# Optimization experiments

Hardware: AMD Instinct MI355X
Metric: run time of the kernel (lower is better)

## Reference

```python
import jax, jax.numpy as jnp
import numpy as np

TEMPERATURE = 10000.0
LN_EPS = 1e-5

def build_freqs(H, W, head_dim):
    # (H*W, head_dim) rotary angles: [theta_h, theta_h, theta_w, theta_w]
    gh, gw = jnp.meshgrid(jnp.arange(H, dtype=jnp.float32), jnp.arange(W, dtype=jnp.float32), indexing='ij')
    dq = head_dim // 4
    freq = 1.0 / (TEMPERATURE ** (jnp.arange(dq, dtype=jnp.float32) / dq))
    th = gh.reshape(-1, 1) * freq[None, :]
    tw = gw.reshape(-1, 1) * freq[None, :]
    return jnp.concatenate([th, th, tw, tw], axis=-1)

def apply_rope(x, freqs):
    # x: (B, nh, N, hd), freqs: (N, hd)
    cos = jnp.cos(freqs)[None, None]
    sin = jnp.sin(freqs)[None, None]
    hd = x.shape[-1]
    x1, x2 = x[..., :hd // 2], x[..., hd // 2:]
    x_rot = jnp.concatenate([-x2, x1], axis=-1)
    return x * cos + x_rot * sin

def setup_inputs() -> dict:
    key = jax.random.key(0)
    ks = jax.random.split(key, 8)
    dim, hidden, B, H, W = 192, 384, 4, 128, 128
    N = H * W
    s = 0.02
    return {
        'x': jax.random.normal(ks[0], (B, N, dim), jnp.float32),
        'in_w': jax.random.normal(ks[1], (hidden, dim), jnp.float32) * s,
        'in_b': jnp.zeros((hidden,), jnp.float32),
        'qkv_w': jax.random.normal(ks[2], (3 * hidden, hidden), jnp.float32) * s,
        'qkv_b': jnp.zeros((3 * hidden,), jnp.float32),
        'lepe_w': jax.random.normal(ks[3], (hidden, 1, 3, 3), jnp.float32) * s,
        'lepe_b': jnp.zeros((hidden,), jnp.float32),
        'ln_g': jnp.ones((hidden,), jnp.float32),
        'ln_b': jnp.zeros((hidden,), jnp.float32),
        'out_w': jax.random.normal(ks[4], (dim, hidden), jnp.float32) * s,
        'out_b': jnp.zeros((dim,), jnp.float32),
        'H': H,
        'W': W,
    }

def reference(x, in_w, in_b, qkv_w, qkv_b, lepe_w, lepe_b, ln_g, ln_b, out_w, out_b, H, W):
    B, N, C = x.shape
    hidden = in_w.shape[0]
    nh = 8
    hd = hidden // nh
    # in_proj: 1x1 conv == per-token linear
    x_seq = jnp.einsum('bnc,hc->bnh', x, in_w) + in_b
    # fused qkv
    qkv = jnp.einsum('bnh,oh->bno', x_seq, qkv_w) + qkv_b
    q, k, v = jnp.split(qkv, 3, axis=-1)
    # LEPE: 3x3 depthwise conv on V in NCHW layout
    v2d = v.transpose(0, 2, 1).reshape(B, hidden, H, W)
    lepe = jax.lax.conv_general_dilated(
        v2d, lepe_w, window_strides=(1, 1), padding=((1, 1), (1, 1)),
        feature_group_count=hidden, dimension_numbers=('NCHW', 'OIHW', 'NCHW'))
    lepe = lepe + lepe_b[None, :, None, None]
    v = v + lepe.reshape(B, hidden, N).transpose(0, 2, 1)
    # split heads -> (B, nh, N, hd)
    q = q.reshape(B, N, nh, hd).transpose(0, 2, 1, 3)
    k = k.reshape(B, N, nh, hd).transpose(0, 2, 1, 3)
    v = v.reshape(B, N, nh, hd).transpose(0, 2, 1, 3)
    freqs = build_freqs(H, W, hd)
    q = apply_rope(q, freqs)
    k = apply_rope(k, freqs)
    # phi = ELU + 1 feature map
    q = jax.nn.elu(q) + 1.0
    k = jax.nn.elu(k) + 1.0
    # linear attention associativity trick
    kv = jnp.einsum('bhnd,bhne->bhde', k, v)
    out = jnp.einsum('bhnd,bhde->bhne', q, kv)
    k_sum = k.sum(axis=2)  # (B, nh, hd)
    denom = jnp.maximum(jnp.einsum('bhnd,bhd->bhn', q, k_sum)[..., None], 1e-6)
    out = out / denom
    out = out.transpose(0, 2, 1, 3).reshape(B, N, hidden)
    # LayerNorm + out_proj
    mu = out.mean(axis=-1, keepdims=True)
    var = out.var(axis=-1, keepdims=True)
    out = (out - mu) * jax.lax.rsqrt(var + LN_EPS) * ln_g + ln_b
    return jnp.einsum('bnh,ch->bnc', out, out_w) + out_b
```

## Files before the change

kernel.cpp:

```cpp
#include <hip/hip_runtime.h>
#include <cstdint>
#include <cstddef>

#define NN_TOK 16384
#define ROWS   65536
#define CDIM   192
#define HID    384
#define NHEAD  8
#define HD     48
#define QKVO   1152

typedef unsigned short ushort_t;
typedef __bf16 bf16x8 __attribute__((ext_vector_type(8)));
typedef float  f32x4  __attribute__((ext_vector_type(4)));

__device__ __forceinline__ ushort_t f2bf(float f) {
  __bf16 h = (__bf16)f;
  ushort_t u;
  __builtin_memcpy(&u, &h, 2);
  return u;
}
__device__ __forceinline__ float bf2f(ushort_t u) {
  return __uint_as_float(((unsigned int)u) << 16);
}

__global__ void cast_x(const float* __restrict__ x, ushort_t* __restrict__ xb, int n8) {
  int i = blockIdx.x * blockDim.x + threadIdx.x;
  if (i >= n8) return;
  const float4* src = (const float4*)(x + (size_t)i * 8);
  float4 f0 = src[0], f1 = src[1];
  uint4 pk;
  pk.x = (unsigned)f2bf(f0.x) | ((unsigned)f2bf(f0.y) << 16);
  pk.y = (unsigned)f2bf(f0.z) | ((unsigned)f2bf(f0.w) << 16);
  pk.z = (unsigned)f2bf(f1.x) | ((unsigned)f2bf(f1.y) << 16);
  pk.w = (unsigned)f2bf(f1.z) | ((unsigned)f2bf(f1.w) << 16);
  *(uint4*)(xb + (size_t)i * 8) = pk;
}

__global__ void combine_w(const float* __restrict__ in_w, const float* __restrict__ in_b,
                          const float* __restrict__ qkv_w, const float* __restrict__ qkv_b,
                          ushort_t* __restrict__ Wcb, float* __restrict__ bc) {
  int o = blockIdx.x;
  int c = threadIdx.x;
  const float* qw = qkv_w + o * HID;
  float s = 0.f;
  for (int m = 0; m < HID; ++m) s += qw[m] * in_w[m * CDIM + c];
  Wcb[o * CDIM + c] = f2bf(s);
  if (c == 0) {
    float sb = qkv_b[o];
    for (int m = 0; m < HID; ++m) sb += qw[m] * in_b[m];
    bc[o] = sb;
  }
}

__global__ void cast_owT(const float* __restrict__ w, ushort_t* __restrict__ wt, int n) {
  int i = blockIdx.x * blockDim.x + threadIdx.x;
  if (i >= n) return;
  int j = i & 7, rest = i >> 3;
  int l15 = rest & 15; rest >>= 4;
  int quad = rest & 3; rest >>= 2;
  int kt = rest % 12, ct = rest / 12;
  int col = ct * 16 + l15, k = kt * 32 + quad * 8 + j;
  wt[i] = f2bf(w[col * HID + k]);
}

__global__ void build_tab(float4* __restrict__ tab4) {
  int i = blockIdx.x * blockDim.x + threadIdx.x;
  if (i >= NN_TOK * 24) return;
  int n = i / 24, dp = i - n * 24;
  int j = dp % 12;
  const float c0 = 1.1073093649624542f;
  float freq = exp2f(-(float)j * c0);
  float fy = (float)(n >> 7), fx = (float)(n & 127);
  float s1, c1, s2, c2;
  sincosf(fy * freq, &s1, &c1);
  sincosf(fx * freq, &s2, &c2);
  tab4[i] = make_float4(c1, s1, c2, s2);
}

template<int BM, int BN, int WM, int WN>
__global__ __launch_bounds__(256) void gemm_qkv(const ushort_t* __restrict__ A, int lda,
                                                const ushort_t* __restrict__ Wb,
                                                const float* __restrict__ bias,
                                                ushort_t* __restrict__ qb,
                                                ushort_t* __restrict__ kTb,
                                                ushort_t* __restrict__ vTb,
                                                int K, int nbx) {
  constexpr int TM = BM / WM / 16;
  constexpr int TN = BN / WN / 16;
  __shared__ __align__(16) ushort_t As[BM][40];
  __shared__ __align__(16) ushort_t Bs[BN][40];
  const int t    = threadIdx.x;
  const int lane = t & 63;
  const int wave = t >> 6;
  const int quad = lane >> 4;
  const int l15  = lane & 15;
  const int wm   = wave / WN, wn = wave % WN;
  const int m_base = wm * (BM / WM);
  const int n_base = wn * (BN / WN);
  const int cpx = gridDim.x >> 3;
  const int id  = blockIdx.x;
  const int swz = (id & 7) * cpx + (id >> 3);
  const int o0  = (swz % nbx) * BN;
  const int n0  = (swz / nbx) * BM;
  f32x4 acc[TM][TN] = {};

  for (int kt = 0; kt < K; kt += 32) {
    for (int c = t; c < BM * 4; c += 256) {
      int row = c >> 2, col8 = (c & 3) * 8;
      *(uint4*)&As[row][col8] = *(const uint4*)(A + (size_t)(n0 + row) * lda + kt + col8);
    }
    for (int c = t; c < BN * 4; c += 256) {
      int row = c >> 2, col8 = (c & 3) * 8;
      *(uint4*)&Bs[row][col8] = *(const uint4*)(Wb + (size_t)(o0 + row) * K + kt + col8);
    }
    __syncthreads();
    bf16x8 af[TM], bfr[TN];
#pragma unroll
    for (int mi = 0; mi < TM; ++mi)
      af[mi] = *(const bf16x8*)&As[m_base + mi * 16 + l15][quad * 8];
#pragma unroll
    for (int ni = 0; ni < TN; ++ni)
      bfr[ni] = *(const bf16x8*)&Bs[n_base + ni * 16 + l15][quad * 8];
#pragma unroll
    for (int mi = 0; mi < TM; ++mi)
#pragma unroll
      for (int ni = 0; ni < TN; ++ni)
        acc[mi][ni] = __builtin_amdgcn_mfma_f32_16x16x32_bf16(af[mi], bfr[ni], acc[mi][ni], 0, 0, 0);
    __syncthreads();
  }
#pragma unroll
  for (int mi = 0; mi < TM; ++mi) {
#pragma unroll
    for (int ni = 0; ni < TN; ++ni) {
      int col = o0 + n_base + ni * 16 + l15;
      float bv = bias[col];
      int rbase = n0 + m_base + mi * 16 + quad * 4;
      if (col < HID) {
#pragma unroll
        for (int r = 0; r < 4; ++r)
          qb[(size_t)(rbase + r) * HID + col] = f2bf(acc[mi][ni][r] + bv);
      } else {
        int co = col - HID;
        ushort_t* dp = kTb;
        if (co >= HID) { co -= HID; dp = vTb; }
        int hh = co / 48, dd = co - hh * 48;
#pragma unroll
        for (int r = 0; r < 4; ++r) {
          int row = rbase + r;
          int bb = row >> 14, n = row & (NN_TOK - 1);
          dp[((size_t)(bb * 8 + hh) * NN_TOK + n) * 48 + dd] = f2bf(acc[mi][ni][r] + bv);
        }
      }
    }
  }
}

__device__ __forceinline__ int fragEl(int pg, int nb, int dd, int nm) {
  return pg * 2200 + nb * 136 + dd * 8 + nm;
}

__global__ __launch_bounds__(256) void kv_partial_k(const ushort_t* __restrict__ kq,
                                                    const ushort_t* __restrict__ vq,
                                                    const float4* __restrict__ tab4,
                                                    const float* __restrict__ lw,
                                                    const float* __restrict__ lb,
                                                    float* __restrict__ part) {
  const int bid   = blockIdx.x;
  const int chunk = bid & 63;
  const int bh    = bid >> 6;
  const int h     = bh & 7;
  const int t     = threadIdx.x;
  const int lane  = t & 63;
  const int wave  = t >> 6;
  __shared__ __align__(16) ushort_t ksR[3 * 2200];
  __shared__ __align__(16) ushort_t vsR[4 * 2200];
  __shared__ __align__(16) float wlds[9][48];
  __shared__ __align__(16) float blds[48];
  float* red = (float*)&ksR[0];
  for (int c = t; c < 432; c += 256) {
    int ch = c / 9, tap = c - ch * 9;
    wlds[tap][ch] = lw[(h * HD + ch) * 9 + tap];
  }
  if (t < 48) blds[t] = lb[h * HD + t];
  for (int c = t; c < 2048; c += 256) {
    int nb = c >> 7, dd = (c >> 3) & 15, nm = c & 7;
    vsR[fragEl(3, nb, dd, nm)] = (dd == 0) ? (ushort_t)0x3F80 : (ushort_t)0;
  }
  __syncthreads();

  const int g  = lane >> 4;
  const int d0 = lane & 15;
  f32x4 acc[3][4] = {};
  const size_t hbase = (size_t)bh * NN_TOK * 48;
  const int nst0 = chunk * 256;

  for (int it = 0; it < 2; ++it) {
    const int nbase = it * 128;
    for (int c = t; c < 384; c += 256) {
      int rr = c / 3, s8 = (c - (c / 3) * 3) * 8;
      int nl = nst0 + nbase + rr;
      const ushort_t* kr = kq + hbase + (size_t)nl * 48;
      uint4 ka = *(const uint4*)(kr + s8);
      uint4 kb = *(const uint4*)(kr + s8 + 24);
      ushort_t ua[8], ub[8];
      *(uint4*)ua = ka; *(uint4*)ub = kb;
      const float4* t4 = tab4 + nl * 24 + s8;
      const int nb = rr >> 3, nm = rr & 7;
#pragma unroll
      for (int jj = 0; jj < 8; ++jj) {
        float4 cs = t4[jj];
        float in1 = bf2f(ua[jj]), in2 = bf2f(ub[jj]);
        float o1 = in1 * cs.x - in2 * cs.y;
        float o2 = in2 * cs.z + in1 * cs.w;
        o1 = (o1 > 0.f) ? o1 + 1.f : __expf(o1);
        o2 = (o2 > 0.f) ? o2 + 1.f : __expf(o2);
        const int d1 = s8 + jj, d2 = s8 + 24 + jj;
        ksR[fragEl(d1 >> 4, nb, d1 & 15, nm)] = f2bf(o1);
        ksR[fragEl(d2 >> 4, nb, d2 & 15, nm)] = f2bf(o2);
      }
    }
    {
      const int y = (nst0 + nbase) >> 7;
      for (int c = t; c < 768; c += 256) {
        int rr = c / 6, gg = c - (c / 6) * 6;
        int x = rr;
        float a8[8], ctr[8];
        *(float4*)&a8[0] = *(const float4*)&blds[gg * 8];
        *(float4*)&a8[4] = *(const float4*)&blds[gg * 8 + 4];
#pragma unroll
        for (int dy = -1; dy <= 1; ++dy) {
#pragma unroll
          for (int dx = -1; dx <= 1; ++dx) {
            int yy = y + dy, xx = x + dx;
            bool inb = ((unsigned)yy < 128u) && ((unsigned)xx < 128u);
            int yc = min(max(yy, 0), 127), xc = min(max(xx, 0), 127);
            const ushort_t* src = vq + hbase + (size_t)((yc << 7) + xc) * 48 + gg * 8;
            uint4 pk = *(const uint4*)src;
            if (!inb) pk = make_uint4(0u, 0u, 0u, 0u);
            const int tap = (dy + 1) * 3 + (dx + 1);
            float wt[8];
            *(float4*)&wt[0] = *(const float4*)&wlds[tap][gg * 8];
            *(float4*)&wt[4] = *(const float4*)&wlds[tap][gg * 8 + 4];
            ushort_t uu[8];
            *(uint4*)uu = pk;
#pragma unroll
            for (int ci = 0; ci < 8; ++ci) {
              float val = bf2f(uu[ci]);
              if (dy == 0 && dx == 0) ctr[ci] = val;
              a8[ci] += wt[ci] * val;
            }
          }
        }
        const int nb = rr >> 3, nm = rr & 7;
#pragma unroll
        for (int ci = 0; ci < 8; ++ci) {
          const int e = gg * 8 + ci;
          vsR[fragEl(e >> 4, nb, e & 15, nm)] = f2bf(ctr[ci] + a8[ci]);
        }
      }
    }
    __syncthreads();
    {
      const int w4 = wave * 4 + g;
      bf16x8 af[3], bfr[4];
#pragma unroll
      for (int dg = 0; dg < 3; ++dg) af[dg]  = *(const bf16x8*)&ksR[fragEl(dg, w4, d0, 0)];
#pragma unroll
      for (int eg = 0; eg < 4; ++eg) bfr[eg] = *(const bf16x8*)&vsR[fragEl(eg, w4, d0, 0)];
#pragma unroll
      for (int dg = 0; dg < 3; ++dg)
#pragma unroll
        for (int eg = 0; eg < 4; ++eg)
          acc[dg][eg] = __builtin_amdgcn_mfma_f32_16x16x32_bf16(af[dg], bfr[eg], acc[dg][eg], 0, 0, 0);
    }
    __syncthreads();
  }
  if (wave == 0) {
#pragma unroll
    for (int dg = 0; dg < 3; ++dg)
#pragma unroll
      for (int eg = 0; eg < 4; ++eg)
#pragma unroll
        for (int r = 0; r < 4; ++r)
          red[(dg * 16 + g * 4 + r) * 64 + eg * 16 + d0] = acc[dg][eg][r];
  }
  __syncthreads();
  for (int w = 1; w < 4; ++w) {
    if (wave == w) {
#pragma unroll
      for (int dg = 0; dg < 3; ++dg)
#pragma unroll
        for (int eg = 0; eg < 4; ++eg)
#pragma unroll
          for (int r = 0; r < 4; ++r)
            red[(dg * 16 + g * 4 + r) * 64 + eg * 16 + d0] += acc[dg][eg][r];
    }
    __syncthreads();
  }
  float* p = part + (size_t)bid * 2352;
  for (int c = t; c < 2352; c += 256) {
    int d = c / 49, e = c - d * 49;
    p[c] = red[d * 64 + e];
  }
}

__global__ void kv_phase2(const float* __restrict__ part, ushort_t* __restrict__ kvT) {
  int bh  = blockIdx.x >> 3;
  int seg = blockIdx.x & 7;
  int t   = threadIdx.x;
  ushort_t* dst = kvT + (size_t)bh * 8192;
  for (int i = seg * 1024 + t; i < (seg + 1) * 1024; i += 256) {
    int rem = i & 4095, e = rem >> 6, d = rem & 63;
    if (d >= 48 || e >= 49) dst[i] = 0;
  }
  int cend = (seg + 1) * 294;
  for (int c = seg * 294 + t; c < cend; c += 256) {
    const float* p = part + (size_t)(bh * 64) * 2352 + c;
    float s = 0.f;
    for (int ch = 0; ch < 64; ++ch) s += p[(size_t)ch * 2352];
    int d = c / 49, e = c - d * 49;
    ushort_t hi = f2bf(s);
    float lo = s - bf2f(hi);
    dst[(size_t)e * 64 + d]        = hi;
    dst[4096 + (size_t)e * 64 + d] = f2bf(lo);
  }
}

__global__ __launch_bounds__(256) void attn_ln_fused(const ushort_t* __restrict__ qb,
                                                     const float4* __restrict__ tab4,
                                                     const ushort_t* __restrict__ kvT,
                                                     const float* __restrict__ ln_g,
                                                     const float* __restrict__ ln_b,
                                                     const ushort_t* __restrict__ owbT,
                                                     const float* __restrict__ out_b,
                                                     float* __restrict__ outp) {
  __shared__ __align__(16) ushort_t qsL[32][392];
  __shared__ __align__(16) float tabL[32][100];
  __shared__ float lnp[4][32][2];
  const int t    = threadIdx.x;
  const int lane = t & 63;
  const int wave = t >> 6;
  const int quad = lane >> 4;
  const int l15  = lane & 15;
  const int row0 = blockIdx.x * 32;
  const int b    = row0 >> 14;
  const int h0   = wave * 2;

  for (int c = t; c < 1536; c += 256) {
    int r = c / 48, seg = c - (c / 48) * 48;
    *(uint4*)&qsL[r][seg * 8] = *(const uint4*)(qb + (size_t)(row0 + r) * HID + seg * 8);
  }
  for (int c = t; c < 768; c += 256) {
    int r = c / 24, dp = c - (c / 24) * 24;
    float4 v = tab4[(size_t)(((row0 + r) & (NN_TOK - 1))) * 24 + dp];
    *(float4*)&tabL[r][dp * 4] = v;
  }
  __syncthreads();

  f32x4 acc[2][2][4] = {};

  float gg[2][3], bb[2][3];
#pragma unroll
  for (int hi = 0; hi < 2; ++hi)
#pragma unroll
    for (int nt = 0; nt < 3; ++nt) {
      int col = (h0 + hi) * 48 + nt * 16 + l15;
      gg[hi][nt] = ln_g[col];
      bb[hi][nt] = ln_b[col];
    }

#pragma unroll
  for (int s = 0; s < 2; ++s) {
    const int d0 = s * 32 + quad * 8;
    bf16x8 bfH[2][4], bfL[2][4];
#pragma unroll
    for (int hi = 0; hi < 2; ++hi) {
      const ushort_t* kb = kvT + (size_t)(b * 8 + h0 + hi) * 8192;
#pragma unroll
      for (int nt = 0; nt < 4; ++nt) {
        bfH[hi][nt] = *(const bf16x8*)(kb + (nt * 16 + l15) * 64 + d0);
        bfL[hi][nt] = *(const bf16x8*)(kb + 4096 + (nt * 16 + l15) * 64 + d0);
      }
    }
    const bool valid = d0 < 48;
    const bool caseA = d0 < 24;
    const int dp0 = caseA ? d0 : d0 - 24;
    bf16x8 af[2][2] = {};
    if (valid) {
      const int dpart = caseA ? d0 + 24 : d0 - 24;
      const int csel  = caseA ? 0 : 2;
      const float sgn = caseA ? -1.f : 1.f;
#pragma unroll
      for (int m = 0; m < 2; ++m) {
        const int r = m * 16 + l15;
        float2 cs[8];
#pragma unroll
        for (int j = 0; j < 8; ++j)
          cs[j] = *(const float2*)&tabL[r][(dp0 + j) * 4 + csel];
#pragma unroll
        for (int hi = 0; hi < 2; ++hi) {
          const ushort_t* qr = &qsL[r][(h0 + hi) * 48];
          uint4 pr = *(const uint4*)(qr + d0);
          uint4 pa = *(const uint4*)(qr + dpart);
          ushort_t up[8], ua[8];
          *(uint4*)up = pr; *(uint4*)ua = pa;
          bf16x8 av;
#pragma unroll
          for (int j = 0; j < 8; ++j) {
            float vp = bf2f(up[j]), va = bf2f(ua[j]);
            float o = vp * cs[j].x + va * (sgn * cs[j].y);
            o = (o > 0.f) ? o + 1.f : __expf(o);
            av[j] = (__bf16)o;
          }
          af[hi][m] = av;
        }
      }
    }
#pragma unroll
    for (int hi = 0; hi < 2; ++hi)
#pragma unroll
      for (int nt = 0; nt < 4; ++nt)
#pragma unroll
        for (int m = 0; m < 2; ++m) {
          acc[hi][m][nt] = __builtin_amdgcn_mfma_f32_16x16x32_bf16(af[hi][m], bfH[hi][nt], acc[hi][m][nt], 0, 0, 0);
          acc[hi][m][nt] = __builtin_amdgcn_mfma_f32_16x16x32_bf16(af[hi][m], bfL[hi][nt], acc[hi][m][nt], 0, 0, 0);
        }
  }

  float rdn[2][2][4];
#pragma unroll
  for (int hi = 0; hi < 2; ++hi)
#pragma unroll
    for (int m = 0; m < 2; ++m)
#pragma unroll
      for (int r = 0; r < 4; ++r) {
        float dn = __shfl(acc[hi][m][3][r], lane & 48);
        rdn[hi][m][r] = 1.f / fmaxf(dn, 1e-6f);
      }
  float s1[2][4] = {}, s2[2][4] = {};
#pragma unroll
  for (int hi = 0; hi < 2; ++hi)
#pragma unroll
    for (int m = 0; m < 2; ++m)
#pragma unroll
      for (int nt = 0; nt < 3; ++nt)
#pragma unroll
        for (int r = 0; r < 4; ++r) {
          float o = acc[hi][m][nt][r] * rdn[hi][m][r];
          acc[hi][m][nt][r] = o;
          s1[m][r] += o;
          s2[m][r] += o * o;
        }
#pragma unroll
  for (int m = 0; m < 2; ++m)
#pragma unroll
    for (int r = 0; r < 4; ++r) {
#pragma unroll
      for (int msk = 1; msk < 16; msk <<= 1) {
        s1[m][r] += __shfl_xor(s1[m][r], msk, 64);
        s2[m][r] += __shfl_xor(s2[m][r], msk, 64);
      }
    }
  if (l15 == 0) {
#pragma unroll
    for (int m = 0; m < 2; ++m)
#pragma unroll
      for (int r = 0; r < 4; ++r) {
        int rr = m * 16 + quad * 4 + r;
        lnp[wave][rr][0] = s1[m][r];
        lnp[wave][rr][1] = s2[m][r];
      }
  }
  __syncthreads();
  float muv[2][4], rsv[2][4];
#pragma unroll
  for (int m = 0; m < 2; ++m)
#pragma unroll
    for (int r = 0; r < 4; ++r) {
      int rr = m * 16 + quad * 4 + r;
      float a  = lnp[0][rr][0] + lnp[1][rr][0] + lnp[2][rr][0] + lnp[3][rr][0];
      float bq = lnp[0][rr][1] + lnp[1][rr][1] + lnp[2][rr][1] + lnp[3][rr][1];
      float mu  = a * (1.f / 384.f);
      float var = bq * (1.f / 384.f) - mu * mu;
      muv[m][r] = mu;
      rsv[m][r] = rsqrtf(var + 1e-5f);
    }
#pragma unroll
  for (int hi = 0; hi < 2; ++hi)
#pragma unroll
    for (int m = 0; m < 2; ++m)
#pragma unroll
      for (int nt = 0; nt < 3; ++nt) {
        int col = (h0 + hi) * 48 + nt * 16 + l15;
#pragma unroll
        for (int r = 0; r < 4; ++r) {
          int rr = m * 16 + quad * 4 + r;
          float v = (acc[hi][m][nt][r] - muv[m][r]) * rsv[m][r] * gg[hi][nt] + bb[hi][nt];
          qsL[rr][col] = f2bf(v);
        }
      }
  __syncthreads();

  f32x4 oac[2][3] = {};
  const int ct0 = wave * 3;
  float obv[3];
#pragma unroll
  for (int nt = 0; nt < 3; ++nt) obv[nt] = out_b[ct0 * 16 + nt * 16 + l15];
#pragma unroll
  for (int kt = 0; kt < 12; ++kt) {
    bf16x8 af2[2];
    af2[0] = *(const bf16x8*)&qsL[l15][kt * 32 + quad * 8];
    af2[1] = *(const bf16x8*)&qsL[16 + l15][kt * 32 + quad * 8];
    bf16x8 bfr2[3];
#pragma unroll
    for (int nt = 0; nt < 3; ++nt)
      bfr2[nt] = *(const bf16x8*)&owbT[(size_t)((((ct0 + nt) * 12 + kt) * 4 + quad) * 16 + l15) * 8];
#pragma unroll
    for (int m2 = 0; m2 < 2; ++m2)
#pragma unroll
      for (int nt = 0; nt < 3; ++nt)
        oac[m2][nt] = __builtin_amdgcn_mfma_f32_16x16x32_bf16(af2[m2], bfr2[nt], oac[m2][nt], 0, 0, 0);
  }
  __syncthreads();
  float* coL = (float*)&qsL[0][0];
#pragma unroll
  for (int m2 = 0; m2 < 2; ++m2)
#pragma unroll
    for (int nt = 0; nt < 3; ++nt) {
      int col = ct0 * 16 + nt * 16 + l15;
#pragma unroll
      for (int r = 0; r < 4; ++r)
        coL[(m2 * 16 + quad * 4 + r) * 196 + col] = oac[m2][nt][r] + obv[nt];
    }
  __syncthreads();
  for (int c = t; c < 1536; c += 256) {
    int r = c / 48, seg = c - (c / 48) * 48;
    *(float4*)(outp + (size_t)(row0 + r) * CDIM + seg * 4) = *(const float4*)&coL[r * 196 + seg * 4];
  }
}

extern "C" void kernel_launch(void* const* d_in, const int* in_sizes, int n_in,
                              void* d_out, int out_size, void* d_ws, size_t ws_size,
                              hipStream_t stream) {
  const float* x      = (const float*)d_in[0];
  const float* in_w   = (const float*)d_in[1];
  const float* in_b   = (const float*)d_in[2];
  const float* qkv_w  = (const float*)d_in[3];
  const float* qkv_b  = (const float*)d_in[4];
  const float* lepe_w = (const float*)d_in[5];
  const float* lepe_b = (const float*)d_in[6];
  const float* ln_g   = (const float*)d_in[7];
  const float* ln_b   = (const float*)d_in[8];
  const float* out_w  = (const float*)d_in[9];
  const float* out_b  = (const float*)d_in[10];
  float* out = (float*)d_out;

  float*    ws     = (float*)d_ws;
  float*    qbF    = ws;
  float*    kTF    = qbF  + (size_t)ROWS * HID / 2;
  float*    vTF    = kTF  + (size_t)ROWS * HID / 2;
  float*    xbF    = vTF  + (size_t)ROWS * HID / 2;
  float*    WcbF   = xbF  + (size_t)ROWS * CDIM / 2;
  float*    bc     = WcbF + (size_t)QKVO * CDIM / 2;
  float*    owbF   = bc   + QKVO;
  float*    tab4F  = owbF + (size_t)CDIM * HID / 2;
  ushort_t* qb     = (ushort_t*)qbF;
  ushort_t* kTb    = (ushort_t*)kTF;
  ushort_t* vTb    = (ushort_t*)vTF;
  ushort_t* xb     = (ushort_t*)xbF;
  float*    part   = xbF;
  ushort_t* kvT    = (ushort_t*)(xbF + (size_t)2048 * 2352);
  ushort_t* Wcb    = (ushort_t*)WcbF;
  ushort_t* owbT   = (ushort_t*)owbF;
  float4*   tab4   = (float4*)tab4F;

  cast_x<<<(ROWS * CDIM / 8 + 255) / 256, 256, 0, stream>>>(x, xb, ROWS * CDIM / 8);
  combine_w<<<QKVO, CDIM, 0, stream>>>(in_w, in_b, qkv_w, qkv_b, Wcb, bc);
  cast_owT<<<(CDIM * HID + 255) / 256, 256, 0, stream>>>(out_w, owbT, CDIM * HID);
  build_tab<<<(NN_TOK * 24 + 255) / 256, 256, 0, stream>>>(tab4);

  gemm_qkv<128, 128, 2, 2><<<4608, 256, 0, stream>>>(
      xb, CDIM, Wcb, bc, qb, kTb, vTb, CDIM, 9);

  kv_partial_k<<<2048, 256, 0, stream>>>(kTb, vTb, tab4, lepe_w, lepe_b, part);
  kv_phase2<<<256, 256, 0, stream>>>(part, kvT);

  attn_ln_fused<<<ROWS / 32, 256, 0, stream>>>(qb, tab4, kvT, ln_g, ln_b, owbT, out_b, out);
}
```

Before: 382.8 us.

## Merge prep kernels into one launch and raise wave priority around MFMA loops

Four small preprocessing kernels (x cast, weight combine, out_w transpose cast, rope table) become one kernel that dispatches on block index, cutting three launches and their inter-kernel gaps. The MFMA inner loops in the GEMM, kv-partial, attention and out-projection kernels are also wrapped with s_setprio(1)/s_setprio(0) to favour waves issuing matrix ops. The merged kernel uses 256 threads for the combine_w part where only 192 are active, and setprio may change wave interleaving in either direction.

```diff
diff --git a/kernel.cpp b/kernel.cpp
--- a/kernel.cpp
+++ b/kernel.cpp
@@ -24,58 +24,62 @@
   return __uint_as_float(((unsigned int)u) << 16);
 }
 
-__global__ void cast_x(const float* __restrict__ x, ushort_t* __restrict__ xb, int n8) {
-  int i = blockIdx.x * blockDim.x + threadIdx.x;
-  if (i >= n8) return;
-  const float4* src = (const float4*)(x + (size_t)i * 8);
-  float4 f0 = src[0], f1 = src[1];
-  uint4 pk;
-  pk.x = (unsigned)f2bf(f0.x) | ((unsigned)f2bf(f0.y) << 16);
-  pk.y = (unsigned)f2bf(f0.z) | ((unsigned)f2bf(f0.w) << 16);
-  pk.z = (unsigned)f2bf(f1.x) | ((unsigned)f2bf(f1.y) << 16);
-  pk.w = (unsigned)f2bf(f1.z) | ((unsigned)f2bf(f1.w) << 16);
-  *(uint4*)(xb + (size_t)i * 8) = pk;
-}
-
-__global__ void combine_w(const float* __restrict__ in_w, const float* __restrict__ in_b,
-                          const float* __restrict__ qkv_w, const float* __restrict__ qkv_b,
-                          ushort_t* __restrict__ Wcb, float* __restrict__ bc) {
-  int o = blockIdx.x;
-  int c = threadIdx.x;
-  const float* qw = qkv_w + o * HID;
-  float s = 0.f;
-  for (int m = 0; m < HID; ++m) s += qw[m] * in_w[m * CDIM + c];
-  Wcb[o * CDIM + c] = f2bf(s);
-  if (c == 0) {
-    float sb = qkv_b[o];
-    for (int m = 0; m < HID; ++m) sb += qw[m] * in_b[m];
-    bc[o] = sb;
-  }
-}
-
-__global__ void cast_owT(const float* __restrict__ w, ushort_t* __restrict__ wt, int n) {
-  int i = blockIdx.x * blockDim.x + threadIdx.x;
-  if (i >= n) return;
-  int j = i & 7, rest = i >> 3;
-  int l15 = rest & 15; rest >>= 4;
-  int quad = rest & 3; rest >>= 2;
-  int kt = rest % 12, ct = rest / 12;
-  int col = ct * 16 + l15, k = kt * 32 + quad * 8 + j;
-  wt[i] = f2bf(w[col * HID + k]);
-}
-
-__global__ void build_tab(float4* __restrict__ tab4) {
-  int i = blockIdx.x * blockDim.x + threadIdx.x;
-  if (i >= NN_TOK * 24) return;
-  int n = i / 24, dp = i - n * 24;
-  int j = dp % 12;
-  const float c0 = 1.1073093649624542f;
-  float freq = exp2f(-(float)j * c0);
-  float fy = (float)(n >> 7), fx = (float)(n & 127);
-  float s1, c1, s2, c2;
-  sincosf(fy * freq, &s1, &c1);
-  sincosf(fx * freq, &s2, &c2);
-  tab4[i] = make_float4(c1, s1, c2, s2);
+#define PREP_CASTX   6144
+#define PREP_COMBW   (PREP_CASTX + 1152)
+#define PREP_OWT     (PREP_COMBW + 288)
+#define PREP_TAB     (PREP_OWT + 1536)
+__global__ __launch_bounds__(256) void prep_all(const float* __restrict__ x, ushort_t* __restrict__ xb,
+                                                const float* __restrict__ in_w, const float* __restrict__ in_b,
+                                                const float* __restrict__ qkv_w, const float* __restrict__ qkv_b,
+                                                ushort_t* __restrict__ Wcb, float* __restrict__ bc,
+                                                const float* __restrict__ out_w, ushort_t* __restrict__ owbT,
+                                                float4* __restrict__ tab4) {
+  const int bid = blockIdx.x;
+  const int t   = threadIdx.x;
+  if (bid < PREP_CASTX) {
+    int i = bid * 256 + t;
+    const float4* src = (const float4*)(x + (size_t)i * 8);
+    float4 f0 = src[0], f1 = src[1];
+    uint4 pk;
+    pk.x = (unsigned)f2bf(f0.x) | ((unsigned)f2bf(f0.y) << 16);
+    pk.y = (unsigned)f2bf(f0.z) | ((unsigned)f2bf(f0.w) << 16);
+    pk.z = (unsigned)f2bf(f1.x) | ((unsigned)f2bf(f1.y) << 16);
+    pk.w = (unsigned)f2bf(f1.z) | ((unsigned)f2bf(f1.w) << 16);
+    *(uint4*)(xb + (size_t)i * 8) = pk;
+  } else if (bid < PREP_COMBW) {
+    int o = bid - PREP_CASTX;
+    int c = t;
+    if (c < CDIM) {
+      const float* qw = qkv_w + o * HID;
+      float s = 0.f;
+      for (int m = 0; m < HID; ++m) s += qw[m] * in_w[m * CDIM + c];
+      Wcb[o * CDIM + c] = f2bf(s);
+      if (c == 0) {
+        float sb = qkv_b[o];
+        for (int m = 0; m < HID; ++m) sb += qw[m] * in_b[m];
+        bc[o] = sb;
+      }
+    }
+  } else if (bid < PREP_OWT) {
+    int i = (bid - PREP_COMBW) * 256 + t;
+    int j = i & 7, rest = i >> 3;
+    int l15 = rest & 15; rest >>= 4;
+    int quad = rest & 3; rest >>= 2;
+    int kt = rest % 12, ct = rest / 12;
+    int col = ct * 16 + l15, k = kt * 32 + quad * 8 + j;
+    owbT[i] = f2bf(out_w[col * HID + k]);
+  } else {
+    int i = (bid - PREP_OWT) * 256 + t;
+    int n = i / 24, dp = i - n * 24;
+    int j = dp % 12;
+    const float c0 = 1.1073093649624542f;
+    float freq = exp2f(-(float)j * c0);
+    float fy = (float)(n >> 7), fx = (float)(n & 127);
+    float s1, c1, s2, c2;
+    sincosf(fy * freq, &s1, &c1);
+    sincosf(fx * freq, &s2, &c2);
+    tab4[i] = make_float4(c1, s1, c2, s2);
+  }
 }
 
 template<int BM, int BN, int WM, int WN>
@@ -122,11 +126,13 @@
 #pragma unroll
     for (int ni = 0; ni < TN; ++ni)
       bfr[ni] = *(const bf16x8*)&Bs[n_base + ni * 16 + l15][quad * 8];
+    __builtin_amdgcn_s_setprio(1);
 #pragma unroll
     for (int mi = 0; mi < TM; ++mi)
 #pragma unroll
       for (int ni = 0; ni < TN; ++ni)
         acc[mi][ni] = __builtin_amdgcn_mfma_f32_16x16x32_bf16(af[mi], bfr[ni], acc[mi][ni], 0, 0, 0);
+    __builtin_amdgcn_s_setprio(0);
     __syncthreads();
   }
 #pragma unroll
@@ -268,11 +274,13 @@
       for (int dg = 0; dg < 3; ++dg) af[dg]  = *(const bf16x8*)&ksR[fragEl(dg, w4, d0, 0)];
 #pragma unroll
       for (int eg = 0; eg < 4; ++eg) bfr[eg] = *(const bf16x8*)&vsR[fragEl(eg, w4, d0, 0)];
+      __builtin_amdgcn_s_setprio(1);
 #pragma unroll
       for (int dg = 0; dg < 3; ++dg)
 #pragma unroll
         for (int eg = 0; eg < 4; ++eg)
           acc[dg][eg] = __builtin_amdgcn_mfma_f32_16x16x32_bf16(af[dg], bfr[eg], acc[dg][eg], 0, 0, 0);
+      __builtin_amdgcn_s_setprio(0);
     }
     __syncthreads();
   }
@@ -417,6 +425,7 @@
         }
       }
     }
+    __builtin_amdgcn_s_setprio(1);
 #pragma unroll
     for (int hi = 0; hi < 2; ++hi)
 #pragma unroll
@@ -426,6 +435,7 @@
           acc[hi][m][nt] = __builtin_amdgcn_mfma_f32_16x16x32_bf16(af[hi][m], bfH[hi][nt], acc[hi][m][nt], 0, 0, 0);
           acc[hi][m][nt] = __builtin_amdgcn_mfma_f32_16x16x32_bf16(af[hi][m], bfL[hi][nt], acc[hi][m][nt], 0, 0, 0);
         }
+    __builtin_amdgcn_s_setprio(0);
   }
 
   float rdn[2][2][4];
@@ -507,6 +517,7 @@
   float obv[3];
 #pragma unroll
   for (int nt = 0; nt < 3; ++nt) obv[nt] = out_b[ct0 * 16 + nt * 16 + l15];
+  __builtin_amdgcn_s_setprio(1);
 #pragma unroll
   for (int kt = 0; kt < 12; ++kt) {
     bf16x8 af2[2];
@@ -522,6 +533,7 @@
       for (int nt = 0; nt < 3; ++nt)
         oac[m2][nt] = __builtin_amdgcn_mfma_f32_16x16x32_bf16(af2[m2], bfr2[nt], oac[m2][nt], 0, 0, 0);
   }
+  __builtin_amdgcn_s_setprio(0);
   __syncthreads();
   float* coL = (float*)&qsL[0][0];
 #pragma unroll
@@ -575,10 +587,8 @@
   ushort_t* owbT   = (ushort_t*)owbF;
   float4*   tab4   = (float4*)tab4F;
 
-  cast_x<<<(ROWS * CDIM / 8 + 255) / 256, 256, 0, stream>>>(x, xb, ROWS * CDIM / 8);
-  combine_w<<<QKVO, CDIM, 0, stream>>>(in_w, in_b, qkv_w, qkv_b, Wcb, bc);
-  cast_owT<<<(CDIM * HID + 255) / 256, 256, 0, stream>>>(out_w, owbT, CDIM * HID);
-  build_tab<<<(NN_TOK * 24 + 255) / 256, 256, 0, stream>>>(tab4);
+  prep_all<<<PREP_TAB, 256, 0, stream>>>(x, xb, in_w, in_b, qkv_w, qkv_b,
+                                         Wcb, bc, out_w, owbT, tab4);
 
   gemm_qkv<128, 128, 2, 2><<<4608, 256, 0, stream>>>(
       xb, CDIM, Wcb, bc, qb, kTb, vTb, CDIM, 9);
```

Measured after the change: 381.4 us. About the same (-0.4%).
